# Optimization experiments

Measured on AMD Instinct MI355X. Metric: run time of the kernel, lower is better.

Reference implementation:

```python
import jax, jax.numpy as jnp
import numpy as np

B, N, DIM = 8, 8192, 256
HEADS, LOCAL_HEADS, WINDOW = 8, 1, 64
HD = DIM // HEADS  # 32
MLP_HIDDEN = 1024
EPS = 1e-5


def layer_norm(x, g, b):
    mu = jnp.mean(x, axis=-1, keepdims=True)
    var = jnp.var(x, axis=-1, keepdims=True)
    return (x - mu) * jax.lax.rsqrt(var + EPS) * g + b


def look_around(t, pad_value=0.0):
    # t: (b, nw, w, ...); concat windows [i-1, i, i+1] -> (b, nw, 3w, ...)
    nw = t.shape[1]
    pads = [(0, 0), (1, 1)] + [(0, 0)] * (t.ndim - 2)
    p = jnp.pad(t, pads, constant_values=pad_value)
    return jnp.concatenate([p[:, i:i + nw] for i in range(3)], axis=2)


def local_attn(q, k, v):
    # lucidrains LocalAttention, causal=False, look_backward=look_forward=1
    # q,k,v: (b_merged, n, d)
    b, n, d = q.shape
    nw = n // WINDOW
    scale = d ** -0.5
    bq = q.reshape(b, nw, WINDOW, d) * scale
    bk = look_around(k.reshape(b, nw, WINDOW, d))  # (b, nw, 3w, d)
    bv = look_around(v.reshape(b, nw, WINDOW, d))
    ticker = jnp.arange(n).reshape(1, nw, WINDOW)
    bq_k = look_around(ticker, pad_value=-1)       # (1, nw, 3w)
    pad_mask = (bq_k == -1)[:, :, None, :]         # (1, nw, 1, 3w)
    dots = jnp.einsum('bnie,bnje->bnij', bq, bk)   # (b, nw, w, 3w)
    dots = jnp.where(pad_mask, -1e9, dots)
    attn = jax.nn.softmax(dots, axis=-1)
    out = jnp.einsum('bnij,bnje->bnie', attn, bv)
    return out.reshape(b, n, d)


def linear_attn(q, k, v):
    # q,k,v: (b, h, n, d)
    d = q.shape[-1]
    qs = jax.nn.softmax(q, axis=-1) * d ** -0.5
    ks = jax.nn.softmax(k, axis=-2)
    ctx = jnp.einsum('bhnd,bhne->bhde', ks, v)     # (b, h, d, d) tiny
    return jnp.einsum('bhnd,bhde->bhne', qs, ctx)


def setup_inputs() -> dict:
    key = jax.random.key(0)
    ks = jax.random.split(key, 8)
    s = 0.02
    return {
        'x': jax.random.normal(ks[0], (B, N, DIM), jnp.float32),
        'norm1_g': jnp.ones((DIM,), jnp.float32),
        'norm1_b': jnp.zeros((DIM,), jnp.float32),
        'Wq': jax.random.normal(ks[1], (DIM, DIM), jnp.float32) * s,
        'Wkv': jax.random.normal(ks[2], (DIM, DIM), jnp.float32) * s,
        'Wproj': jax.random.normal(ks[3], (DIM, DIM), jnp.float32) * s,
        'bproj': jnp.zeros((DIM,), jnp.float32),
        'norm2_g': jnp.ones((DIM,), jnp.float32),
        'norm2_b': jnp.zeros((DIM,), jnp.float32),
        'W1': jax.random.normal(ks[4], (MLP_HIDDEN, DIM), jnp.float32) * s,
        'b1': jnp.zeros((MLP_HIDDEN,), jnp.float32),
        'W2': jax.random.normal(ks[5], (DIM, MLP_HIDDEN), jnp.float32) * s,
        'b2': jnp.zeros((DIM,), jnp.float32),
    }


def reference(x, norm1_g, norm1_b, Wq, Wkv, Wproj, bproj, norm2_g, norm2_b, W1, b1, W2, b2):
    b, n, c = x.shape
    h = layer_norm(x, norm1_g, norm1_b)
    q = h @ Wq.T
    kv = h @ Wkv.T  # k and v share the same projection in the original code
    split_heads = lambda t: t.reshape(b, n, HEADS, HD).transpose(0, 2, 1, 3)
    q, k, v = split_heads(q), split_heads(kv), split_heads(kv)
    lq, gq = q[:, :LOCAL_HEADS], q[:, LOCAL_HEADS:]
    lk, gk = k[:, :LOCAL_HEADS], k[:, LOCAL_HEADS:]
    lv, gv = v[:, :LOCAL_HEADS], v[:, LOCAL_HEADS:]
    lout = local_attn(lq.reshape(b * LOCAL_HEADS, n, HD),
                      lk.reshape(b * LOCAL_HEADS, n, HD),
                      lv.reshape(b * LOCAL_HEADS, n, HD)).reshape(b, LOCAL_HEADS, n, HD)
    gout = linear_attn(gq, gk, gv)
    attn = jnp.concatenate([lout, gout], axis=1)   # (b, H, n, hd)
    y = attn.transpose(0, 2, 1, 3).reshape(b, n, c) @ Wproj.T + bproj
    x = x + y
    h2 = layer_norm(x, norm2_g, norm2_b)
    m = jax.nn.gelu(h2 @ W1.T + b1, approximate=False) @ W2.T + b2
    return x + m
```

## Files before the change

kernel.cpp:

```cpp
#include <hip/hip_runtime.h>
#include <hip/hip_bf16.h>

typedef __bf16 bf16;
typedef __bf16 bf16x8 __attribute__((ext_vector_type(8)));
typedef float f32x4 __attribute__((ext_vector_type(4)));

__device__ __forceinline__ void gld16(const void* g, void* l) {
  __builtin_amdgcn_global_load_lds((const __attribute__((address_space(1))) void*)g,
                                   (__attribute__((address_space(3))) void*)l, 16, 0, 0);
}

__global__ void cvt_weights(const float* __restrict__ wq, const float* __restrict__ wkv,
                            const float* __restrict__ wp, const float* __restrict__ w1,
                            const float* __restrict__ w2,
                            bf16* __restrict__ wqkv, bf16* __restrict__ wpb,
                            bf16* __restrict__ w1b, bf16* __restrict__ w2b) {
  int i = blockIdx.x * 256 + threadIdx.x;
  if (i < 65536) wqkv[i] = (bf16)wq[i];
  else if (i < 131072) wqkv[i] = (bf16)wkv[i - 65536];
  else if (i < 196608) wpb[i - 131072] = (bf16)wp[i - 131072];
  else if (i < 458752) w1b[i - 196608] = (bf16)w1[i - 196608];
  else if (i < 720896) w2b[i - 458752] = (bf16)w2[i - 458752];
}

__launch_bounds__(256)
__global__ void ln_kernel(const float* __restrict__ x, const float* __restrict__ g,
                          const float* __restrict__ b, bf16* __restrict__ out) {
  const int row = blockIdx.x * 4 + (threadIdx.x >> 6);
  const int lane = threadIdx.x & 63;
  const float4 v = ((const float4*)(x + (long)row * 256))[lane];
  float s = v.x + v.y + v.z + v.w;
#pragma unroll
  for (int o = 1; o < 64; o <<= 1) s += __shfl_xor(s, o);
  const float mu = s * (1.f / 256.f);
  const float dx = v.x - mu, dy = v.y - mu, dz = v.z - mu, dw = v.w - mu;
  float q = dx * dx + dy * dy + dz * dz + dw * dw;
#pragma unroll
  for (int o = 1; o < 64; o <<= 1) q += __shfl_xor(q, o);
  const float rstd = rsqrtf(q * (1.f / 256.f) + 1e-5f);
  const float4 gg = ((const float4*)g)[lane];
  const float4 bb = ((const float4*)b)[lane];
  union { bf16 h[4]; uint2 u; } pk;
  pk.h[0] = (bf16)(dx * rstd * gg.x + bb.x);
  pk.h[1] = (bf16)(dy * rstd * gg.y + bb.y);
  pk.h[2] = (bf16)(dz * rstd * gg.z + bb.z);
  pk.h[3] = (bf16)(dw * rstd * gg.w + bb.w);
  *(uint2*)(out + (long)row * 256 + lane * 4) = pk.u;
}

template <int EPI, int NCG, int NCHUNK, int THREADS, int MSPLIT>
__launch_bounds__(THREADS, (THREADS == 512) ? 4 : 2)
__global__ void gemm_pb(const bf16* __restrict__ A, const bf16* __restrict__ Bw,
                        void* C, const float* __restrict__ bias,
                        const float* res, int ldC) {
  constexpr int WAVES = THREADS / 64;
  constexpr int WR = (THREADS == 512) ? 2 : 1;
  constexpr int WC = WAVES / WR;
  constexpr int FN = (THREADS == 512) ? 2 : 1;
  constexpr int FM = 64 / WR / 16;
  constexpr int COLS = WC * FN * 16;
  constexpr int KK = NCHUNK * 128;
  constexpr int ITER = 64 * 128 * 2 / (THREADS * 16);
  constexpr int TILES = 65536 / MSPLIT / 64;
  constexpr int CHB = 64 * 128 * 2;
  constexpr int BSZ = (EPI == 1) ? 64 * COLS * 4 : 64 * COLS * 2;
  constexpr int NST = (EPI == 1) ? 12 : 2;
  constexpr int NBLK = NCG * MSPLIT;
  __shared__ char smem[3 * CHB + BSZ];
  const int tid = threadIdx.x;
  const int w = tid >> 6, lane = tid & 63;
  const int l15 = lane & 15, l4 = lane >> 4;
  const int wrow = w & (WR - 1), wcol = w / WR;
  const int bid = blockIdx.x;
  const int slot = (bid & 7) * (NBLK / 8) + (bid >> 3);
  const int cg = slot % NCG;
  const long strip0 = (long)(slot / NCG) * (65536 / MSPLIT);

  const bf16* Bl = Bw + (long)(cg * COLS + wcol * FN * 16 + l15) * KK + l4 * 8;
  bf16x8 Breg[NCHUNK][4][FN];
#pragma unroll
  for (int c = 0; c < NCHUNK; ++c)
#pragma unroll
    for (int kl = 0; kl < 4; ++kl)
#pragma unroll
      for (int fn = 0; fn < FN; ++fn)
        Breg[c][kl][fn] = *(const bf16x8*)(Bl + (long)fn * 16 * KK + c * 128 + kl * 32);

  float bias_r[FN];
  if constexpr (EPI == 2) {
#pragma unroll
    for (int fn = 0; fn < FN; ++fn)
      bias_r[fn] = bias[cg * COLS + wcol * FN * 16 + fn * 16 + l15];
  }

  auto stage = [&](int m, int c, int buf) {
#pragma unroll
    for (int it = 0; it < ITER; ++it) {
      const int p = it * (THREADS * 16) + tid * 16;
      const int row = p >> 8;
      const int colb = (p & 255) ^ ((row & 7) << 4);
      gld16((const char*)A + ((strip0 + m * 64 + row) * KK + c * 128) * 2 + colb,
            smem + buf * CHB + it * (THREADS * 16) + w * 1024);
    }
  };

  f32x4 acc[FM][FN] = {};
  stage(0, 0, 0);
  stage(0, 1, 1);

  for (int m = 0; m < TILES; ++m) {
#pragma unroll
    for (int c = 0; c < NCHUNK; ++c) {
      const int s = m * NCHUNK + c;
      if (m == 0 || c >= 2) {
        asm volatile("s_waitcnt vmcnt(%0)" ::"i"(ITER) : "memory");
      } else {
        asm volatile("s_waitcnt vmcnt(%0)" ::"i"(ITER + NST) : "memory");
      }
      __syncthreads();
      {
        int c2 = c + 2, m2 = m;
        if (c2 >= NCHUNK) { c2 -= NCHUNK; ++m2; }
        if (m2 < TILES) stage(m2, c2, (s + 2) % 3);
      }
      const char* Ab = smem + (s % 3) * CHB;
#pragma unroll
      for (int kl = 0; kl < 4; ++kl) {
        bf16x8 af[FM];
#pragma unroll
        for (int fm = 0; fm < FM; ++fm) {
          const int arow = wrow * (64 / WR) + fm * 16 + l15;
          af[fm] = *(const bf16x8*)(Ab + arow * 256 + ((kl * 64 + l4 * 16) ^ ((l15 & 7) << 4)));
        }
#pragma unroll
        for (int fm = 0; fm < FM; ++fm)
#pragma unroll
          for (int fn = 0; fn < FN; ++fn)
            acc[fm][fn] = __builtin_amdgcn_mfma_f32_16x16x32_bf16(af[fm], Breg[c][kl][fn],
                                                                  acc[fm][fn], 0, 0, 0);
      }
      if (c == NCHUNK - 1) {
        if constexpr (EPI == 1) {
          float* fb = (float*)(smem + 3 * CHB);
#pragma unroll
          for (int fm = 0; fm < FM; ++fm)
#pragma unroll
            for (int fn = 0; fn < FN; ++fn)
#pragma unroll
              for (int r = 0; r < 4; ++r)
                fb[(wrow * (64 / WR) + fm * 16 + l4 * 4 + r) * COLS +
                   wcol * FN * 16 + fn * 16 + l15] = acc[fm][fn][r];
          __syncthreads();
#pragma unroll
          for (int it = 0; it < 64 * COLS * 4 / (THREADS * 16); ++it) {
            const int off = it * (THREADS * 16) + tid * 16;
            const int row = off / (COLS * 4);
            const int colb = off % (COLS * 4);
            const long gb = ((strip0 + m * 64 + row) * ldC + cg * COLS) * 4 + colb;
            float4 v = *(const float4*)(smem + 3 * CHB + off);
            const float4 rr = *(const float4*)((const char*)res + gb);
            const float4 bv = *(const float4*)((const char*)bias + cg * COLS * 4 + colb);
            v.x += rr.x + bv.x; v.y += rr.y + bv.y;
            v.z += rr.z + bv.z; v.w += rr.w + bv.w;
            *(float4*)((char*)C + gb) = v;
          }
        } else {
          bf16* bb = (bf16*)(smem + 3 * CHB);
#pragma unroll
          for (int fm = 0; fm < FM; ++fm)
#pragma unroll
            for (int fn = 0; fn < FN; ++fn)
#pragma unroll
              for (int r = 0; r < 4; ++r) {
                float v = acc[fm][fn][r];
                if constexpr (EPI == 2) {
                  v += bias_r[fn];
                  v = 0.5f * v * (1.f + erff(v * 0.70710678118654752f));
                }
                bb[(wrow * (64 / WR) + fm * 16 + l4 * 4 + r) * COLS +
                   wcol * FN * 16 + fn * 16 + l15] = (bf16)v;
              }
          __syncthreads();
#pragma unroll
          for (int it = 0; it < 64 * COLS * 2 / (THREADS * 16); ++it) {
            const int off = it * (THREADS * 16) + tid * 16;
            const int row = off / (COLS * 2);
            const int colb = off % (COLS * 2);
            *(uint4*)((char*)C + ((strip0 + m * 64 + row) * ldC + cg * COLS) * 2 + colb) =
                *(const uint4*)(smem + 3 * CHB + off);
          }
        }
#pragma unroll
        for (int fm = 0; fm < FM; ++fm)
#pragma unroll
          for (int fn = 0; fn < FN; ++fn)
            acc[fm][fn] = f32x4{0.f, 0.f, 0.f, 0.f};
      }
    }
  }
}

__launch_bounds__(256)
__global__ void lattn_kernel(const bf16* __restrict__ qkv, bf16* __restrict__ attn) {
  const int j = blockIdx.x, b = blockIdx.y;
  const int tid = threadIdx.x, w = tid >> 6, lane = tid & 63;
  __shared__ bf16 Qs[64 * 40];
  __shared__ bf16 Ks[192 * 40];
  __shared__ bf16 Kt[32 * 200];
  __shared__ bf16 Ps[4][16 * 200];
  const float scale = 0.17677669529663687f;
  const long base = (long)b * 8192 + (long)j * 64;
  for (int i = tid; i < 64 * 32; i += 256) {
    const int r = i >> 5, d = i & 31;
    Qs[r * 40 + d] = (bf16)((float)qkv[(base + r) * 512 + d] * scale);
  }
  for (int i = tid; i < 192 * 32; i += 256) {
    const int c = i >> 5, d = i & 31;
    const long tc = (long)j * 64 - 64 + c;
    float kv = 0.f;
    if (tc >= 0 && tc < 8192) kv = (float)qkv[((long)b * 8192 + tc) * 512 + 256 + d];
    const bf16 kb = (bf16)kv;
    Ks[c * 40 + d] = kb;
    Kt[d * 200 + c] = kb;
  }
  __syncthreads();
  const int l15 = lane & 15, l4 = lane >> 4;
  const bf16x8 aq = *(const bf16x8*)(Qs + (w * 16 + l15) * 40 + l4 * 8);
  const f32x4 zz = {0.f, 0.f, 0.f, 0.f};
  f32x4 S[12];
#pragma unroll
  for (int fn = 0; fn < 12; ++fn) {
    const bf16x8 bk = *(const bf16x8*)(Ks + (fn * 16 + l15) * 40 + l4 * 8);
    S[fn] = __builtin_amdgcn_mfma_f32_16x16x32_bf16(aq, bk, zz, 0, 0, 0);
  }
#pragma unroll
  for (int fn = 0; fn < 12; ++fn) {
    const long tc = (long)j * 64 - 64 + fn * 16 + l15;
    if (tc < 0 || tc >= 8192) { S[fn][0] = -1e9f; S[fn][1] = -1e9f; S[fn][2] = -1e9f; S[fn][3] = -1e9f; }
  }
  float sinv[4];
#pragma unroll
  for (int r = 0; r < 4; ++r) {
    float m = -1e30f;
#pragma unroll
    for (int fn = 0; fn < 12; ++fn) m = fmaxf(m, S[fn][r]);
#pragma unroll
    for (int o = 1; o < 16; o <<= 1) m = fmaxf(m, __shfl_xor(m, o));
    float s = 0.f;
#pragma unroll
    for (int fn = 0; fn < 12; ++fn) { const float e = __expf(S[fn][r] - m); S[fn][r] = e; s += e; }
#pragma unroll
    for (int o = 1; o < 16; o <<= 1) s += __shfl_xor(s, o);
    sinv[r] = 1.f / s;
  }
#pragma unroll
  for (int fn = 0; fn < 12; ++fn)
#pragma unroll
    for (int r = 0; r < 4; ++r)
      Ps[w][(l4 * 4 + r) * 200 + fn * 16 + l15] = (bf16)(S[fn][r] * sinv[r]);
  __syncthreads();
  f32x4 O[2] = {};
#pragma unroll
  for (int ks = 0; ks < 6; ++ks) {
    const bf16x8 ap = *(const bf16x8*)(Ps[w] + l15 * 200 + ks * 32 + l4 * 8);
#pragma unroll
    for (int fe = 0; fe < 2; ++fe) {
      const bf16x8 bv = *(const bf16x8*)(Kt + (fe * 16 + l15) * 200 + ks * 32 + l4 * 8);
      O[fe] = __builtin_amdgcn_mfma_f32_16x16x32_bf16(ap, bv, O[fe], 0, 0, 0);
    }
  }
#pragma unroll
  for (int fe = 0; fe < 2; ++fe)
#pragma unroll
    for (int r = 0; r < 4; ++r)
      attn[(base + w * 16 + l4 * 4 + r) * 256 + fe * 16 + l15] = (bf16)O[fe][r];
}

__launch_bounds__(256)
__global__ void ctx_kernel(const bf16* __restrict__ qkv, float* __restrict__ ctx,
                           float* __restrict__ S) {
  const int bh = blockIdx.x;
  const int b = bh / 7, h = bh % 7 + 1;
  const int tid = threadIdx.x;
  const int w = tid >> 6, lane = tid & 63;
  const int l15 = lane & 15, l4 = lane >> 4;
  __shared__ bf16 evT[32 * 264];
  __shared__ bf16 kT[48 * 264];
  __shared__ float red[4][32 * 48];
  const long n0 = (long)blockIdx.y * 256;
  const bf16* kp = qkv + ((long)b * 8192 + n0 + tid) * 512 + 256 + h * 32;
  bf16x8 kv[4];
#pragma unroll
  for (int c = 0; c < 4; ++c) kv[c] = *(const bf16x8*)(kp + c * 8);
#pragma unroll
  for (int i = 0; i < 16; ++i)
    kT[(32 + i) * 264 + tid] = (i == 0) ? (bf16)1.0f : (bf16)0.0f;
#pragma unroll
  for (int c = 0; c < 4; ++c)
#pragma unroll
    for (int j = 0; j < 8; ++j) {
      const int d = c * 8 + j;
      evT[d * 264 + tid] = (bf16)__expf((float)kv[c][j]);
      kT[d * 264 + tid] = kv[c][j];
    }
  __syncthreads();
  f32x4 acc[2][3] = {};
#pragma unroll
  for (int ks = 0; ks < 2; ++ks) {
    const int ncol = w * 64 + ks * 32 + l4 * 8;
    bf16x8 af[2], bb[3];
#pragma unroll
    for (int fm = 0; fm < 2; ++fm) af[fm] = *(const bf16x8*)(evT + (fm * 16 + l15) * 264 + ncol);
#pragma unroll
    for (int fe = 0; fe < 3; ++fe) bb[fe] = *(const bf16x8*)(kT + (fe * 16 + l15) * 264 + ncol);
#pragma unroll
    for (int fm = 0; fm < 2; ++fm)
#pragma unroll
      for (int fe = 0; fe < 3; ++fe)
        acc[fm][fe] = __builtin_amdgcn_mfma_f32_16x16x32_bf16(af[fm], bb[fe], acc[fm][fe], 0, 0, 0);
  }
#pragma unroll
  for (int fm = 0; fm < 2; ++fm)
#pragma unroll
    for (int fe = 0; fe < 3; ++fe)
#pragma unroll
      for (int r = 0; r < 4; ++r)
        red[w][(fm * 16 + l4 * 4 + r) * 48 + fe * 16 + l15] = acc[fm][fe][r];
  __syncthreads();
  for (int i = tid; i < 32 * 48; i += 256) {
    const float v = red[0][i] + red[1][i] + red[2][i] + red[3][i];
    const int d = i / 48, e = i - d * 48;
    if (e < 32) atomicAdd(ctx + (long)bh * 1024 + d * 32 + e, v);
    else if (e == 32) atomicAdd(S + bh * 32 + d, v);
  }
}

__launch_bounds__(256)
__global__ void lout_kernel(const bf16* __restrict__ qkv, const float* __restrict__ S,
                            const float* __restrict__ ctx, bf16* __restrict__ attn) {
  const int bh = blockIdx.x;
  const int b = bh / 7, h = bh % 7 + 1;
  const int tid = threadIdx.x;
  const int w = tid >> 6, lane = tid & 63;
  const int l15 = lane & 15, l4 = lane >> 4;
  __shared__ bf16 qs[256 * 40];
  __shared__ bf16 C2t[32 * 40];
  const long n0 = (long)blockIdx.y * 256;
  for (int i = tid; i < 1024; i += 256) {
    const int e = i >> 5, d = i & 31;
    C2t[e * 40 + d] = (bf16)(ctx[(long)bh * 1024 + d * 32 + e] / S[bh * 32 + d]);
  }
  const bf16* qp = qkv + ((long)b * 8192 + n0 + tid) * 512 + h * 32;
  bf16x8 qv[4];
#pragma unroll
  for (int c = 0; c < 4; ++c) qv[c] = *(const bf16x8*)(qp + c * 8);
  float qf[32];
#pragma unroll
  for (int c = 0; c < 4; ++c)
#pragma unroll
    for (int j = 0; j < 8; ++j) qf[c * 8 + j] = (float)qv[c][j];
  float m = qf[0];
#pragma unroll
  for (int d = 1; d < 32; ++d) m = fmaxf(m, qf[d]);
  float s = 0.f;
#pragma unroll
  for (int d = 0; d < 32; ++d) { qf[d] = __expf(qf[d] - m); s += qf[d]; }
  const float f = 0.17677669529663687f / s;
#pragma unroll
  for (int c = 0; c < 4; ++c) {
    bf16x8 o;
#pragma unroll
    for (int j = 0; j < 8; ++j) o[j] = (bf16)(qf[c * 8 + j] * f);
    *(bf16x8*)(qs + tid * 40 + c * 8) = o;
  }
  __syncthreads();
  f32x4 acc[4][2] = {};
  bf16x8 bfr[2];
#pragma unroll
  for (int fe = 0; fe < 2; ++fe) bfr[fe] = *(const bf16x8*)(C2t + (fe * 16 + l15) * 40 + l4 * 8);
#pragma unroll
  for (int fm = 0; fm < 4; ++fm) {
    const bf16x8 af = *(const bf16x8*)(qs + (w * 64 + fm * 16 + l15) * 40 + l4 * 8);
#pragma unroll
    for (int fe = 0; fe < 2; ++fe)
      acc[fm][fe] = __builtin_amdgcn_mfma_f32_16x16x32_bf16(af, bfr[fe], acc[fm][fe], 0, 0, 0);
  }
#pragma unroll
  for (int fm = 0; fm < 4; ++fm)
#pragma unroll
    for (int fe = 0; fe < 2; ++fe)
#pragma unroll
      for (int r = 0; r < 4; ++r)
        attn[((long)b * 8192 + n0 + w * 64 + fm * 16 + l4 * 4 + r) * 256 + h * 32 + fe * 16 + l15]
            = (bf16)acc[fm][fe][r];
}

extern "C" void kernel_launch(void* const* d_in, const int* in_sizes, int n_in,
                              void* d_out, int out_size, void* d_ws, size_t ws_size,
                              hipStream_t stream) {
  const float* x     = (const float*)d_in[0];
  const float* n1g   = (const float*)d_in[1];
  const float* n1b   = (const float*)d_in[2];
  const float* Wq    = (const float*)d_in[3];
  const float* Wkv   = (const float*)d_in[4];
  const float* Wproj = (const float*)d_in[5];
  const float* bproj = (const float*)d_in[6];
  const float* n2g   = (const float*)d_in[7];
  const float* n2b   = (const float*)d_in[8];
  const float* W1    = (const float*)d_in[9];
  const float* b1    = (const float*)d_in[10];
  const float* W2    = (const float*)d_in[11];
  const float* b2    = (const float*)d_in[12];
  float* out = (float*)d_out;
  char* ws = (char*)d_ws;

  bf16* wqkv   = (bf16*)(ws + 0);
  bf16* wprojb = (bf16*)(ws + 262144);
  bf16* w1b    = (bf16*)(ws + 393216);
  bf16* w2b    = (bf16*)(ws + 917504);
  float* Sbuf  = (float*)(ws + 1441792);
  float* ctx   = (float*)(ws + 1448960);
  bf16* hbuf   = (bf16*)(ws + 1685504);
  bf16* qkv    = (bf16*)(ws + 35239936);
  bf16* hidden = qkv;

  cvt_weights<<<2816, 256, 0, stream>>>(Wq, Wkv, Wproj, W1, W2, wqkv, wprojb, w1b, w2b);
  ln_kernel<<<16384, 256, 0, stream>>>(x, n1g, n1b, hbuf);
  gemm_pb<0, 4, 2, 512, 128><<<512, 512, 0, stream>>>(hbuf, wqkv, qkv, nullptr, nullptr, 512);
  hipMemsetAsync(Sbuf, 0, 7168 + 229376, stream);
  lattn_kernel<<<dim3(128, 8), 256, 0, stream>>>(qkv, hbuf);
  ctx_kernel<<<dim3(56, 32), 256, 0, stream>>>(qkv, ctx, Sbuf);
  lout_kernel<<<dim3(56, 32), 256, 0, stream>>>(qkv, Sbuf, ctx, hbuf);
  gemm_pb<1, 2, 2, 512, 256><<<512, 512, 0, stream>>>(hbuf, wprojb, out, bproj, x, 256);
  ln_kernel<<<16384, 256, 0, stream>>>(out, n2g, n2b, hbuf);
  gemm_pb<2, 8, 2, 512, 64><<<512, 512, 0, stream>>>(hbuf, w1b, hidden, b1, nullptr, 1024);
  gemm_pb<1, 4, 8, 256, 256><<<1024, 256, 0, stream>>>(hidden, w2b, out, b2, out, 256);
}
```

Before: 332.4 us.

## Replace MLP down-projection GEMM with a dedicated kernel streaming B from global

Adds a specialized gemm_mlp2 kernel for the K=1024 second MLP GEMM. Instead of holding all B weights in registers, it double-buffers B fragments per K-chunk via global loads and uses explicit vmcnt waits to overlap them with the triple-buffered A staging. Each block now covers a 128-column group with wider per-wave fragments (FN=2, 4 row fragments), and the residual add is done in place. The generic gemm_pb template is also changed to always use the 512-thread layout parameters. Hand-tuned waitcnt values are fragile, and the narrower column grouping may change how A is reused.

New measurement: 355.2 us. +6.8%, slower.

```diff
diff --git a/kernel.cpp b/kernel.cpp
--- a/kernel.cpp
+++ b/kernel.cpp
@@ -49,14 +49,14 @@
 }
 
 template <int EPI, int NCG, int NCHUNK, int THREADS, int MSPLIT>
-__launch_bounds__(THREADS, (THREADS == 512) ? 4 : 2)
+__launch_bounds__(THREADS, 4)
 __global__ void gemm_pb(const bf16* __restrict__ A, const bf16* __restrict__ Bw,
                         void* C, const float* __restrict__ bias,
                         const float* res, int ldC) {
   constexpr int WAVES = THREADS / 64;
-  constexpr int WR = (THREADS == 512) ? 2 : 1;
+  constexpr int WR = 2;
   constexpr int WC = WAVES / WR;
-  constexpr int FN = (THREADS == 512) ? 2 : 1;
+  constexpr int FN = 2;
   constexpr int FM = 64 / WR / 16;
   constexpr int COLS = WC * FN * 16;
   constexpr int KK = NCHUNK * 128;
@@ -92,6 +92,7 @@
     for (int fn = 0; fn < FN; ++fn)
       bias_r[fn] = bias[cg * COLS + wcol * FN * 16 + fn * 16 + l15];
   }
+  asm volatile("" ::: "memory");
 
   auto stage = [&](int m, int c, int buf) {
 #pragma unroll
@@ -196,6 +197,99 @@
           for (int fn = 0; fn < FN; ++fn)
             acc[fm][fn] = f32x4{0.f, 0.f, 0.f, 0.f};
       }
+    }
+  }
+}
+
+__launch_bounds__(256, 3)
+__global__ void gemm_mlp2(const bf16* __restrict__ A, const bf16* __restrict__ Bw,
+                          float* __restrict__ C, const float* __restrict__ bias) {
+  constexpr int TILES = 2, NCHUNK = 8, ITER = 4, CHB = 64 * 128 * 2;
+  __shared__ char smem[3 * CHB];
+  const int tid = threadIdx.x;
+  const int w = tid >> 6, lane = tid & 63;
+  const int l15 = lane & 15, l4 = lane >> 4;
+  const int bid = blockIdx.x;
+  const int slot = (bid & 7) * 128 + (bid >> 3);
+  const int cg = slot & 1;
+  const long strip0 = (long)(slot >> 1) * 128;
+  const bf16* Bl = Bw + (long)(cg * 128 + w * 32 + l15) * 1024 + l4 * 8;
+  const float bias0 = bias[cg * 128 + w * 32 + l15];
+  const float bias1 = bias[cg * 128 + w * 32 + 16 + l15];
+
+  auto stage = [&](int m, int c, int buf) {
+#pragma unroll
+    for (int it = 0; it < ITER; ++it) {
+      const int p = it * 4096 + tid * 16;
+      const int row = p >> 8;
+      const int colb = (p & 255) ^ ((row & 7) << 4);
+      gld16((const char*)A + ((strip0 + m * 64 + row) * 1024 + c * 128) * 2 + colb,
+            smem + buf * CHB + it * 4096 + w * 1024);
+    }
+  };
+  auto loadB = [&](int c, bf16x8 (&Bn)[2][4]) {
+#pragma unroll
+    for (int fn = 0; fn < 2; ++fn)
+#pragma unroll
+      for (int kl = 0; kl < 4; ++kl)
+        Bn[fn][kl] = *(const bf16x8*)(Bl + (long)fn * 16 * 1024 + c * 128 + kl * 32);
+  };
+
+  bf16x8 B0[2][4], B1[2][4];
+  f32x4 acc[4][2] = {};
+  stage(0, 0, 0);
+  stage(0, 1, 1);
+  loadB(0, B0);
+
+  auto body = [&](int m, int c, bf16x8 (&Bu)[2][4], bf16x8 (&Bn)[2][4]) {
+    const int s = m * NCHUNK + c;
+    if (s == 0)
+      asm volatile("s_waitcnt vmcnt(12)" ::: "memory");
+    else if (s == TILES * NCHUNK - 1)
+      asm volatile("s_waitcnt vmcnt(16)" ::: "memory");
+    else
+      asm volatile("s_waitcnt vmcnt(20)" ::: "memory");
+    __syncthreads();
+    {
+      int c2 = c + 2, m2 = m;
+      if (c2 >= NCHUNK) { c2 -= NCHUNK; ++m2; }
+      if (m2 < TILES) stage(m2, c2, (s + 2) % 3);
+    }
+    loadB((c + 1) & 7, Bn);
+    const char* Ab = smem + (s % 3) * CHB;
+#pragma unroll
+    for (int kl = 0; kl < 4; ++kl) {
+      bf16x8 af[4];
+#pragma unroll
+      for (int fm = 0; fm < 4; ++fm)
+        af[fm] = *(const bf16x8*)(Ab + (fm * 16 + l15) * 256 + ((kl * 64 + l4 * 16) ^ ((l15 & 7) << 4)));
+#pragma unroll
+      for (int fm = 0; fm < 4; ++fm) {
+        acc[fm][0] = __builtin_amdgcn_mfma_f32_16x16x32_bf16(af[fm], Bu[0][kl], acc[fm][0], 0, 0, 0);
+        acc[fm][1] = __builtin_amdgcn_mfma_f32_16x16x32_bf16(af[fm], Bu[1][kl], acc[fm][1], 0, 0, 0);
+      }
+    }
+    if (c == NCHUNK - 1) {
+#pragma unroll
+      for (int fm = 0; fm < 4; ++fm)
+#pragma unroll
+        for (int r = 0; r < 4; ++r) {
+          const long row = strip0 + m * 64 + fm * 16 + l4 * 4 + r;
+          const long i0 = row * 256 + cg * 128 + w * 32 + l15;
+          C[i0]      = acc[fm][0][r] + bias0 + C[i0];
+          C[i0 + 16] = acc[fm][1][r] + bias1 + C[i0 + 16];
+          acc[fm][0][r] = 0.f;
+          acc[fm][1][r] = 0.f;
+        }
+      asm volatile("s_waitcnt vmcnt(12)" ::: "memory");
+    }
+  };
+
+  for (int m = 0; m < TILES; ++m) {
+#pragma unroll
+    for (int cp = 0; cp < NCHUNK; cp += 2) {
+      body(m, cp, B0, B1);
+      body(m, cp + 1, B1, B0);
     }
   }
 }
@@ -434,5 +528,5 @@
   gemm_pb<1, 2, 2, 512, 256><<<512, 512, 0, stream>>>(hbuf, wprojb, out, bproj, x, 256);
   ln_kernel<<<16384, 256, 0, stream>>>(out, n2g, n2b, hbuf);
   gemm_pb<2, 8, 2, 512, 64><<<512, 512, 0, stream>>>(hbuf, w1b, hidden, b1, nullptr, 1024);
-  gemm_pb<1, 4, 8, 256, 256><<<1024, 256, 0, stream>>>(hidden, w2b, out, b2, out, 256);
-}
+  gemm_mlp2<<<1024, 256, 0, stream>>>(hidden, w2b, out, b2);
+}
```

## Fuse MLP up-projection, GELU and down-projection into one kernel

Applied to the files above, without the earlier changes.

Replaces the two MLP GEMM launches with a single kernel that keeps a 64-row strip of the normed activations in LDS. It computes the 1024-wide hidden layer in 128-column chunks with bias and exact GELU, then accumulates the down-projection into registers. This avoids writing and re-reading the 64 MB bf16 hidden tensor in global memory. Weights are now read straight from global/L2 on every chunk with no LDS staging or pipelining, which risks exposed load latency. The generic GEMM template is also simplified to a fixed warp layout.

New measurement: 337.1 us. Within noise of the previous version (+1.4%).

```diff
diff --git a/kernel.cpp b/kernel.cpp
--- a/kernel.cpp
+++ b/kernel.cpp
@@ -49,14 +49,14 @@
 }
 
 template <int EPI, int NCG, int NCHUNK, int THREADS, int MSPLIT>
-__launch_bounds__(THREADS, (THREADS == 512) ? 4 : 2)
+__launch_bounds__(THREADS, 4)
 __global__ void gemm_pb(const bf16* __restrict__ A, const bf16* __restrict__ Bw,
                         void* C, const float* __restrict__ bias,
                         const float* res, int ldC) {
   constexpr int WAVES = THREADS / 64;
-  constexpr int WR = (THREADS == 512) ? 2 : 1;
+  constexpr int WR = 2;
   constexpr int WC = WAVES / WR;
-  constexpr int FN = (THREADS == 512) ? 2 : 1;
+  constexpr int FN = 2;
   constexpr int FM = 64 / WR / 16;
   constexpr int COLS = WC * FN * 16;
   constexpr int KK = NCHUNK * 128;
@@ -92,6 +92,7 @@
     for (int fn = 0; fn < FN; ++fn)
       bias_r[fn] = bias[cg * COLS + wcol * FN * 16 + fn * 16 + l15];
   }
+  asm volatile("" ::: "memory");
 
   auto stage = [&](int m, int c, int buf) {
 #pragma unroll
@@ -198,6 +199,101 @@
       }
     }
   }
+}
+
+__launch_bounds__(256, 2)
+__global__ void gemm_mlp(const bf16* __restrict__ A, const bf16* __restrict__ W1b,
+                         const bf16* __restrict__ W2b, float* __restrict__ C,
+                         const float* __restrict__ b1, const float* __restrict__ b2) {
+  __shared__ bf16 h2s[64 * 256];
+  __shared__ bf16 ht[64 * 128];
+  const int tid = threadIdx.x;
+  const int w = tid >> 6, lane = tid & 63;
+  const int l15 = lane & 15, l4 = lane >> 4;
+  const int slot = ((blockIdx.x & 7) << 7) | (blockIdx.x >> 3);
+  const long strip0 = (long)slot * 64;
+  const int c0 = w * 64;
+
+#pragma unroll
+  for (int it = 0; it < 8; ++it) {
+    const int p = it * 4096 + tid * 16;
+    const int row = p >> 9;
+    const int colb = (p & 511) ^ ((row & 7) << 4);
+    gld16((const char*)A + ((strip0 + row) * 256) * 2 + colb,
+          (char*)h2s + it * 4096 + w * 1024);
+  }
+  float b2r[4];
+#pragma unroll
+  for (int fn = 0; fn < 4; ++fn) b2r[fn] = b2[c0 + fn * 16 + l15];
+  asm volatile("s_waitcnt vmcnt(0)" ::: "memory");
+  __syncthreads();
+
+  f32x4 acc2[4][4] = {};
+  for (int hc = 0; hc < 8; ++hc) {
+    f32x4 acc1[4][2] = {};
+    const bf16* W1p = W1b + ((long)hc * 128 + w * 32 + l15) * 256 + l4 * 8;
+    const float b1r0 = b1[hc * 128 + w * 32 + l15];
+    const float b1r1 = b1[hc * 128 + w * 32 + 16 + l15];
+#pragma unroll
+    for (int kl = 0; kl < 8; ++kl) {
+      const bf16x8 bf0 = *(const bf16x8*)(W1p + kl * 32);
+      const bf16x8 bf1 = *(const bf16x8*)(W1p + 16 * 256 + kl * 32);
+      bf16x8 af[4];
+#pragma unroll
+      for (int fm = 0; fm < 4; ++fm)
+        af[fm] = *(const bf16x8*)((const char*)h2s + (fm * 16 + l15) * 512 +
+                                  ((kl * 64 + l4 * 16) ^ ((l15 & 7) << 4)));
+#pragma unroll
+      for (int fm = 0; fm < 4; ++fm) {
+        acc1[fm][0] = __builtin_amdgcn_mfma_f32_16x16x32_bf16(af[fm], bf0, acc1[fm][0], 0, 0, 0);
+        acc1[fm][1] = __builtin_amdgcn_mfma_f32_16x16x32_bf16(af[fm], bf1, acc1[fm][1], 0, 0, 0);
+      }
+    }
+#pragma unroll
+    for (int fm = 0; fm < 4; ++fm)
+#pragma unroll
+      for (int fn = 0; fn < 2; ++fn)
+#pragma unroll
+        for (int r = 0; r < 4; ++r) {
+          const int row = fm * 16 + l4 * 4 + r;
+          const int col = w * 32 + fn * 16 + l15;
+          float t = acc1[fm][fn][r] + (fn ? b1r1 : b1r0);
+          t = 0.5f * t * (1.f + erff(t * 0.70710678118654752f));
+          *(bf16*)((char*)ht + row * 256 + ((col * 2) ^ ((row & 7) << 4))) = (bf16)t;
+        }
+    __syncthreads();
+    const bf16* W2p = W2b + ((long)c0 + l15) * 1024 + hc * 128 + l4 * 8;
+#pragma unroll
+    for (int kl = 0; kl < 4; ++kl) {
+      bf16x8 bg[4];
+#pragma unroll
+      for (int fn = 0; fn < 4; ++fn)
+        bg[fn] = *(const bf16x8*)(W2p + (long)fn * 16 * 1024 + kl * 32);
+      bf16x8 ag[4];
+#pragma unroll
+      for (int fm = 0; fm < 4; ++fm)
+        ag[fm] = *(const bf16x8*)((const char*)ht + (fm * 16 + l15) * 256 +
+                                  ((kl * 64 + l4 * 16) ^ ((l15 & 7) << 4)));
+#pragma unroll
+      for (int fm = 0; fm < 4; ++fm)
+#pragma unroll
+        for (int fn = 0; fn < 4; ++fn)
+          acc2[fm][fn] = __builtin_amdgcn_mfma_f32_16x16x32_bf16(ag[fm], bg[fn],
+                                                                 acc2[fm][fn], 0, 0, 0);
+    }
+    __syncthreads();
+  }
+
+#pragma unroll
+  for (int fm = 0; fm < 4; ++fm)
+#pragma unroll
+    for (int fn = 0; fn < 4; ++fn)
+#pragma unroll
+      for (int r = 0; r < 4; ++r) {
+        const long row = strip0 + fm * 16 + l4 * 4 + r;
+        const long idx = row * 256 + c0 + fn * 16 + l15;
+        C[idx] = C[idx] + acc2[fm][fn][r] + b2r[fn];
+      }
 }
 
 __launch_bounds__(256)
@@ -422,7 +518,6 @@
   float* ctx   = (float*)(ws + 1448960);
   bf16* hbuf   = (bf16*)(ws + 1685504);
   bf16* qkv    = (bf16*)(ws + 35239936);
-  bf16* hidden = qkv;
 
   cvt_weights<<<2816, 256, 0, stream>>>(Wq, Wkv, Wproj, W1, W2, wqkv, wprojb, w1b, w2b);
   ln_kernel<<<16384, 256, 0, stream>>>(x, n1g, n1b, hbuf);
@@ -433,6 +528,5 @@
   lout_kernel<<<dim3(56, 32), 256, 0, stream>>>(qkv, Sbuf, ctx, hbuf);
   gemm_pb<1, 2, 2, 512, 256><<<512, 512, 0, stream>>>(hbuf, wprojb, out, bproj, x, 256);
   ln_kernel<<<16384, 256, 0, stream>>>(out, n2g, n2b, hbuf);
-  gemm_pb<2, 8, 2, 512, 64><<<512, 512, 0, stream>>>(hbuf, w1b, hidden, b1, nullptr, 1024);
-  gemm_pb<1, 4, 8, 256, 256><<<1024, 256, 0, stream>>>(hidden, w2b, out, b2, out, 256);
-}
+  gemm_mlp<<<1024, 256, 0, stream>>>(hbuf, w1b, w2b, out, b1, b2);
+}
```
